# Optimization experiments

Measured on AMD Instinct MI355X. Metric: run time of the kernel, lower is better.

Reference implementation:

```python
import jax, jax.numpy as jnp
import numpy as np

B, H, S, D = 4, 16, 1024, 64
MAX_REL = 128
VOCAB = 2 * MAX_REL + 1  # relative-position vocabulary


def setup_inputs() -> dict:
    key = jax.random.key(0)
    k1, k2, k3, k4 = jax.random.split(key, 4)
    tensor = jax.random.normal(k1, (B, H, S, D), dtype=jnp.float32)
    rel_keys_emb = jax.random.normal(k2, (VOCAB, D), dtype=jnp.float32) * 0.02
    rel_values_emb = jax.random.normal(k3, (VOCAB, D), dtype=jnp.float32) * 0.02
    # nn.Parameter initialized xavier_uniform_ on shape (1, H, 1, 1)
    bias = jax.random.uniform(k4, (1, H, 1, 1), dtype=jnp.float32, minval=-1.0, maxval=1.0)
    return {
        "tensor": tensor,
        "rel_keys_emb": rel_keys_emb,
        "rel_values_emb": rel_values_emb,
        "bias": bias,
        "max_relative_position": MAX_REL,
    }


def reference(tensor, rel_keys_emb, rel_values_emb, bias, max_relative_position):
    # forward(tensor, is_key=True, transpose=False)
    seq_len = tensor.shape[2]
    r = jnp.arange(seq_len)
    dist = jnp.clip(r[None, :] - r[:, None], -max_relative_position, max_relative_position)
    idx = dist + max_relative_position          # [S, S] in [0, 2*max_rel]
    rel_emb = rel_keys_emb[idx]                 # [S, S, D] gathered table
    # original: [S, B*H, D] @ [S, D, S] -> [S, B*H, S] -> [B, H, S, S]
    scores = jnp.einsum('bhsd,std->bhst', tensor, rel_emb)
    return scores + bias
```

## Files before the change

kernel.cpp:

```cpp
#include <hip/hip_runtime.h>


constexpr int S_ = 1024;
constexpr int D_ = 64;
constexpr int CP = 280;
constexpr int ROWS = 64;
constexpr int CHUNKS = 2;

typedef __attribute__((ext_vector_type(8))) short short8;
typedef __attribute__((ext_vector_type(4))) float f32x4;

__device__ __forceinline__ unsigned short f2bf(float x) {
  unsigned u = __float_as_uint(x);
  return (unsigned short)((u + 0x7fffu + ((u >> 16) & 1u)) >> 16);
}
__device__ __forceinline__ f32x4 ld4(const float* p) {
  return *reinterpret_cast<const f32x4*>(p);
}
__device__ __forceinline__ short8 pack8(f32x4 a, f32x4 b) {
  short8 r;
  r[0] = (short)f2bf(a.x); r[1] = (short)f2bf(a.y);
  r[2] = (short)f2bf(a.z); r[3] = (short)f2bf(a.w);
  r[4] = (short)f2bf(b.x); r[5] = (short)f2bf(b.y);
  r[6] = (short)f2bf(b.z); r[7] = (short)f2bf(b.w);
  return r;
}

__global__ __launch_bounds__(256, 1)
void relpos_v8(const float* __restrict__ tensor,
               const float* __restrict__ relk,
               const float* __restrict__ bias,
               float* __restrict__ out) {
  __shared__ __align__(16) unsigned short c_lds[ROWS * CP];

  const int tid  = threadIdx.x;
  const int lane = tid & 63;
  const int w    = tid >> 6;
  const int l15  = lane & 15;
  const int l4   = lane >> 4;
  const int r0   = 16 * w + l4 * 4;
  const int pb   = 4 * (l4 & 1);

  for (int ch = 0; ch < CHUNKS; ++ch) {
    const int cid = blockIdx.x * CHUNKS + ch;
    const int bh  = cid >> 4;
    const int s0  = (cid & 15) * ROWS;
    const float bv = bias[bh & 15];

    const float* xrow = tensor + ((size_t)(bh * S_ + s0 + 16 * w + l15)) * D_ + l4 * 8;
    short8 a0 = pack8(ld4(xrow),      ld4(xrow + 4));
    short8 a1 = pack8(ld4(xrow + 32), ld4(xrow + 36));

    if (ch) __syncthreads();

#pragma unroll 2
    for (int nt = 0; nt < 17; ++nt) {
      const int vcol = 16 * nt + l15;
      const int erow = vcol > 256 ? 256 : vcol;
      const float* ep = relk + (size_t)erow * D_ + l4 * 8;
      short8 b0 = pack8(ld4(ep),      ld4(ep + 4));
      short8 b1 = pack8(ld4(ep + 32), ld4(ep + 36));
      f32x4 acc = {0.f, 0.f, 0.f, 0.f};
      acc = __builtin_amdgcn_mfma_f32_16x16x32_bf16(a0, b0, acc, 0, 0, 0);
      acc = __builtin_amdgcn_mfma_f32_16x16x32_bf16(a1, b1, acc, 0, 0, 0);
      if (vcol <= 256) {
#pragma unroll
        for (int i = 0; i < 4; ++i)
          c_lds[(r0 + i) * CP + pb + i + 8 + vcol] = f2bf(acc[i] + bv);
      }
      if (l15 == 0 && nt == 0) {
#pragma unroll
        for (int i = 0; i < 4; ++i) {
          const unsigned short cv = f2bf(acc[i] + bv);
          const int pad = pb + i;
          for (int j = 0; j <= pad + 7; ++j) c_lds[(r0 + i) * CP + j] = cv;
        }
      }
      if (l15 == 0 && nt == 16) {
#pragma unroll
        for (int i = 0; i < 4; ++i) {
          const unsigned short cv = f2bf(acc[i] + bv);
          const int pad = pb + i;
          for (int j = pad + 265; j < CP; ++j) c_lds[(r0 + i) * CP + j] = cv;
        }
      }
    }
    __syncthreads();

    float* obase = out + ((size_t)(bh * S_ + s0)) * (size_t)S_;
    const int mc = 136 - s0;
#pragma unroll 8
    for (int it = 0; it < 32; ++it) {
      const int idx = it * 256 + tid;
      const int rl  = idx >> 7;
      const int t0  = (idx & 127) << 3;
      int m0 = t0 + (rl & 7) + mc - rl;
      m0 = m0 < 0 ? 0 : (m0 > 272 ? 272 : m0);
      const uint4 q = *reinterpret_cast<const uint4*>(&c_lds[rl * CP + m0]);
      f32x4 o0, o1;
      o0.x = __uint_as_float(q.x << 16);
      o0.y = __uint_as_float(q.x & 0xffff0000u);
      o0.z = __uint_as_float(q.y << 16);
      o0.w = __uint_as_float(q.y & 0xffff0000u);
      o1.x = __uint_as_float(q.z << 16);
      o1.y = __uint_as_float(q.z & 0xffff0000u);
      o1.z = __uint_as_float(q.w << 16);
      o1.w = __uint_as_float(q.w & 0xffff0000u);
      float* p = obase + ((size_t)rl << 10) + t0;
      *reinterpret_cast<f32x4*>(p)     = o0;
      *reinterpret_cast<f32x4*>(p + 4) = o1;
    }
  }
}

extern "C" void kernel_launch(void* const* d_in, const int* in_sizes, int n_in,
                              void* d_out, int out_size, void* d_ws, size_t ws_size,
                              hipStream_t stream) {
  const float* tensor = (const float*)d_in[0];
  const float* relk   = (const float*)d_in[1];
  const float* bias   = (const float*)d_in[3];
  float* out          = (float*)d_out;

  dim3 grid(512);
  dim3 block(256);
  relpos_v8<<<grid, block, 0, stream>>>(tensor, relk, bias, out);
}
```

Measured before the change: 72.97 us.

## Split work into one chunk per block and use system-scope streaming stores

Launches one block per 64-row chunk instead of looping over two chunks per block, and raises launch bounds to allow four blocks per CU for more overlap. Output stores are replaced with inline-asm global_store_dwordx4 carrying sc0 sc1 cache-policy bits, aiming to stream the large output past caches. The coherence bits might instead add write overhead, and extra blocks repeat the embedding-table loads.

```diff
diff --git a/kernel.cpp b/kernel.cpp
--- a/kernel.cpp
+++ b/kernel.cpp
@@ -3,9 +3,8 @@
 
 constexpr int S_ = 1024;
 constexpr int D_ = 64;
+constexpr int BQ = 64;
 constexpr int CP = 280;
-constexpr int ROWS = 64;
-constexpr int CHUNKS = 2;
 
 typedef __attribute__((ext_vector_type(8))) short short8;
 typedef __attribute__((ext_vector_type(4))) float f32x4;
@@ -25,91 +24,90 @@
   r[6] = (short)f2bf(b.z); r[7] = (short)f2bf(b.w);
   return r;
 }
+__device__ __forceinline__ void store_sys(float* __restrict__ base, unsigned byte_off, f32x4 v) {
+  asm volatile("global_store_dwordx4 %0, %1, %2 sc0 sc1"
+               :: "v"(byte_off), "v"(v), "s"(base)
+               : "memory");
+}
 
-__global__ __launch_bounds__(256, 1)
-void relpos_v8(const float* __restrict__ tensor,
-               const float* __restrict__ relk,
-               const float* __restrict__ bias,
-               float* __restrict__ out) {
-  __shared__ __align__(16) unsigned short c_lds[ROWS * CP];
+__global__ __launch_bounds__(256, 4)
+void relpos_v12(const float* __restrict__ tensor,
+                const float* __restrict__ relk,
+                const float* __restrict__ bias,
+                float* __restrict__ out) {
+  __shared__ __align__(16) unsigned short c_lds[BQ * CP];
 
   const int tid  = threadIdx.x;
   const int lane = tid & 63;
   const int w    = tid >> 6;
+  const int bh   = blockIdx.x >> 4;
+  const int s0   = (blockIdx.x & 15) * BQ;
+  const int h    = bh & 15;
   const int l15  = lane & 15;
   const int l4   = lane >> 4;
   const int r0   = 16 * w + l4 * 4;
   const int pb   = 4 * (l4 & 1);
 
-  for (int ch = 0; ch < CHUNKS; ++ch) {
-    const int cid = blockIdx.x * CHUNKS + ch;
-    const int bh  = cid >> 4;
-    const int s0  = (cid & 15) * ROWS;
-    const float bv = bias[bh & 15];
-
-    const float* xrow = tensor + ((size_t)(bh * S_ + s0 + 16 * w + l15)) * D_ + l4 * 8;
-    short8 a0 = pack8(ld4(xrow),      ld4(xrow + 4));
-    short8 a1 = pack8(ld4(xrow + 32), ld4(xrow + 36));
-
-    if (ch) __syncthreads();
+  const float* xrow = tensor + ((size_t)(bh * S_ + s0 + 16 * w + l15)) * D_ + l4 * 8;
+  short8 a0 = pack8(ld4(xrow),      ld4(xrow + 4));
+  short8 a1 = pack8(ld4(xrow + 32), ld4(xrow + 36));
+  const float bv = bias[h];
 
 #pragma unroll 2
-    for (int nt = 0; nt < 17; ++nt) {
-      const int vcol = 16 * nt + l15;
-      const int erow = vcol > 256 ? 256 : vcol;
-      const float* ep = relk + (size_t)erow * D_ + l4 * 8;
-      short8 b0 = pack8(ld4(ep),      ld4(ep + 4));
-      short8 b1 = pack8(ld4(ep + 32), ld4(ep + 36));
-      f32x4 acc = {0.f, 0.f, 0.f, 0.f};
-      acc = __builtin_amdgcn_mfma_f32_16x16x32_bf16(a0, b0, acc, 0, 0, 0);
-      acc = __builtin_amdgcn_mfma_f32_16x16x32_bf16(a1, b1, acc, 0, 0, 0);
-      if (vcol <= 256) {
+  for (int nt = 0; nt < 17; ++nt) {
+    const int vcol = 16 * nt + l15;
+    const int erow = vcol > 256 ? 256 : vcol;
+    const float* ep = relk + (size_t)erow * D_ + l4 * 8;
+    short8 b0 = pack8(ld4(ep),      ld4(ep + 4));
+    short8 b1 = pack8(ld4(ep + 32), ld4(ep + 36));
+    f32x4 acc = {0.f, 0.f, 0.f, 0.f};
+    acc = __builtin_amdgcn_mfma_f32_16x16x32_bf16(a0, b0, acc, 0, 0, 0);
+    acc = __builtin_amdgcn_mfma_f32_16x16x32_bf16(a1, b1, acc, 0, 0, 0);
+    if (vcol <= 256) {
 #pragma unroll
-        for (int i = 0; i < 4; ++i)
-          c_lds[(r0 + i) * CP + pb + i + 8 + vcol] = f2bf(acc[i] + bv);
-      }
-      if (l15 == 0 && nt == 0) {
+      for (int i = 0; i < 4; ++i)
+        c_lds[(r0 + i) * CP + pb + i + 8 + vcol] = f2bf(acc[i] + bv);
+    }
+    if (l15 == 0 && nt == 0) {
 #pragma unroll
-        for (int i = 0; i < 4; ++i) {
-          const unsigned short cv = f2bf(acc[i] + bv);
-          const int pad = pb + i;
-          for (int j = 0; j <= pad + 7; ++j) c_lds[(r0 + i) * CP + j] = cv;
-        }
-      }
-      if (l15 == 0 && nt == 16) {
-#pragma unroll
-        for (int i = 0; i < 4; ++i) {
-          const unsigned short cv = f2bf(acc[i] + bv);
-          const int pad = pb + i;
-          for (int j = pad + 265; j < CP; ++j) c_lds[(r0 + i) * CP + j] = cv;
-        }
+      for (int i = 0; i < 4; ++i) {
+        const unsigned short cv = f2bf(acc[i] + bv);
+        const int pad = pb + i;
+        for (int j = 0; j <= pad + 7; ++j) c_lds[(r0 + i) * CP + j] = cv;
       }
     }
-    __syncthreads();
+    if (l15 == 0 && nt == 16) {
+#pragma unroll
+      for (int i = 0; i < 4; ++i) {
+        const unsigned short cv = f2bf(acc[i] + bv);
+        const int pad = pb + i;
+        for (int j = pad + 265; j < CP; ++j) c_lds[(r0 + i) * CP + j] = cv;
+      }
+    }
+  }
+  __syncthreads();
 
-    float* obase = out + ((size_t)(bh * S_ + s0)) * (size_t)S_;
-    const int mc = 136 - s0;
+  float* obase = out + ((size_t)(bh * S_ + s0)) * (size_t)S_;
+  const int mc = 136 - s0;
 #pragma unroll 8
-    for (int it = 0; it < 32; ++it) {
-      const int idx = it * 256 + tid;
-      const int rl  = idx >> 7;
-      const int t0  = (idx & 127) << 3;
-      int m0 = t0 + (rl & 7) + mc - rl;
-      m0 = m0 < 0 ? 0 : (m0 > 272 ? 272 : m0);
-      const uint4 q = *reinterpret_cast<const uint4*>(&c_lds[rl * CP + m0]);
-      f32x4 o0, o1;
-      o0.x = __uint_as_float(q.x << 16);
-      o0.y = __uint_as_float(q.x & 0xffff0000u);
-      o0.z = __uint_as_float(q.y << 16);
-      o0.w = __uint_as_float(q.y & 0xffff0000u);
-      o1.x = __uint_as_float(q.z << 16);
-      o1.y = __uint_as_float(q.z & 0xffff0000u);
-      o1.z = __uint_as_float(q.w << 16);
-      o1.w = __uint_as_float(q.w & 0xffff0000u);
-      float* p = obase + ((size_t)rl << 10) + t0;
-      *reinterpret_cast<f32x4*>(p)     = o0;
-      *reinterpret_cast<f32x4*>(p + 4) = o1;
-    }
+  for (int it = 0; it < 32; ++it) {
+    const int idx = it * 256 + tid;
+    const int rl  = idx >> 7;
+    const int t0  = (idx & 127) << 3;
+    int m0 = t0 + (rl & 7) + mc - rl;
+    m0 = m0 < 0 ? 0 : (m0 > 272 ? 272 : m0);
+    const uint4 q = *reinterpret_cast<const uint4*>(&c_lds[rl * CP + m0]);
+    f32x4 o0, o1;
+    o0.x = __uint_as_float(q.x << 16);
+    o0.y = __uint_as_float(q.x & 0xffff0000u);
+    o0.z = __uint_as_float(q.y << 16);
+    o0.w = __uint_as_float(q.y & 0xffff0000u);
+    o1.x = __uint_as_float(q.z << 16);
+    o1.y = __uint_as_float(q.z & 0xffff0000u);
+    o1.z = __uint_as_float(q.w << 16);
+    o1.w = __uint_as_float(q.w & 0xffff0000u);
+    store_sys(obase, (unsigned)idx * 32u,       o0);
+    store_sys(obase, (unsigned)idx * 32u + 16u, o1);
   }
 }
 
@@ -121,7 +119,8 @@
   const float* bias   = (const float*)d_in[3];
   float* out          = (float*)d_out;
 
-  dim3 grid(512);
+  const int B = 4, H = 16;
+  dim3 grid(B * H * (S_ / BQ));
   dim3 block(256);
-  relpos_v8<<<grid, block, 0, stream>>>(tensor, relk, bias, out);
+  relpos_v12<<<grid, block, 0, stream>>>(tensor, relk, bias, out);
 }
```

Result: slower. 142.5 us (+95.2%).
